# Performance work log

Hardware: AMD Instinct MI355X
Metric: run time of the kernel (lower is better)

Reference implementation:

```python
import jax, jax.numpy as jnp
import numpy as np

B, H = 65536, 512


def setup_inputs() -> dict:
    key = jax.random.key(0)
    ks = jax.random.split(key, 10)
    s = 1.0 / np.sqrt(H)  # torch nn.Linear default init range
    uni = lambda k, shape: jax.random.uniform(k, shape, jnp.float32, -s, s)
    return {
        "inputs": jax.random.normal(ks[0], (B, H), jnp.float32),
        "short_term_memory": jax.random.normal(ks[1], (B, H), jnp.float32),
        "Wf": uni(ks[2], (H, H)), "bf": uni(ks[3], (H,)),
        "Wi": uni(ks[4], (H, H)), "bi": uni(ks[5], (H,)),
        "Wg": uni(ks[6], (H, H)), "bg": uni(ks[7], (H,)),
        "Wo": uni(ks[8], (H, H)), "bo": uni(ks[9], (H,)),
    }


def reference(inputs, short_term_memory, Wf, bf, Wi, bi, Wg, bg, Wo, bo):
    z = inputs + short_term_memory  # [B, H]
    # ForgetGate: OVERWRITES long-term memory (previous cell state never read).
    c = jax.nn.sigmoid(z @ Wf.T + bf)
    # InputGate: c += sigmoid(...) * tanh(...)
    c = c + jax.nn.sigmoid(z @ Wi.T + bi) * jnp.tanh(z @ Wg.T + bg)
    # OutputGate: h = tanh(c) * sigmoid(...)
    h = jnp.tanh(c) * jax.nn.sigmoid(z @ Wo.T + bo)
    return jnp.stack((c, h))  # [2, B, H]: new long-term and short-term memory
```

## Files before the change

### kernel.cpp

```cpp
#include <hip/hip_runtime.h>

typedef __bf16 bf16x8 __attribute__((ext_vector_type(8)));
typedef float  f32x4  __attribute__((ext_vector_type(4)));

#define LOG2E 1.4426950408889634f

static __device__ __forceinline__ float fexp2(float x) { return __builtin_amdgcn_exp2f(x); }
static __device__ __forceinline__ float frcp(float x)  { return __builtin_amdgcn_rcpf(x); }
static __device__ __forceinline__ float fsigmoid(float x) { return frcp(1.0f + fexp2(-LOG2E * x)); }
static __device__ __forceinline__ float ftanh(float x)    { return 2.0f * frcp(1.0f + fexp2(-2.0f * LOG2E * x)) - 1.0f; }

__global__ __launch_bounds__(256) void wpack(const float* __restrict__ Wf,
                                             const float* __restrict__ Wi,
                                             const float* __restrict__ Wg,
                                             const float* __restrict__ Wo,
                                             __bf16* __restrict__ Wp)
{
    int idx = blockIdx.x * 256 + threadIdx.x;
    int kg  = idx & 63;
    int j   = (idx >> 6) & 511;
    int g   = idx >> 15;
    const float* src = (g == 0) ? Wf : (g == 1) ? Wi : (g == 2) ? Wg : Wo;
    const float4* s4 = (const float4*)(src + j * 512 + kg * 8);
    float4 v0 = s4[0], v1 = s4[1];
    bf16x8 o;
    o[0] = (__bf16)v0.x; o[1] = (__bf16)v0.y; o[2] = (__bf16)v0.z; o[3] = (__bf16)v0.w;
    o[4] = (__bf16)v1.x; o[5] = (__bf16)v1.y; o[6] = (__bf16)v1.z; o[7] = (__bf16)v1.w;
    int cn = j >> 4;
    int ks = kg >> 2;
    int lt = (j & 15) + (kg & 3) * 16;
    size_t dst = ((size_t)(((g * 32 + cn) * 16 + ks) * 64 + lt)) * 8;
    *(bf16x8*)(Wp + dst) = o;
}

__global__ __launch_bounds__(512, 2) void lstm_main(
    const float* __restrict__ xin, const float* __restrict__ stm,
    const __bf16* __restrict__ Wp,
    const float* __restrict__ bfv, const float* __restrict__ biv,
    const float* __restrict__ bgv, const float* __restrict__ bov,
    float* __restrict__ out)
{
    __shared__ unsigned char zs[131072];
    const int tid  = threadIdx.x;
    const int lane = tid & 63;
    const int wv   = tid >> 6;
    const int l15  = lane & 15;
    const int lq   = lane >> 4;
    const int row0 = blockIdx.x * 128;

    {
        const float* xb = xin + (size_t)row0 * 512;
        const float* sb = stm + (size_t)row0 * 512;
        #pragma unroll
        for (int it = 0; it < 16; ++it) {
            int idx = it * 512 + tid;
            int row = idx >> 6;
            int kg  = idx & 63;
            const float4* x4 = (const float4*)(xb + row * 512 + kg * 8);
            const float4* s4 = (const float4*)(sb + row * 512 + kg * 8);
            float4 a0 = x4[0], a1 = x4[1];
            float4 b0 = s4[0], b1 = s4[1];
            bf16x8 p;
            p[0] = (__bf16)(a0.x + b0.x); p[1] = (__bf16)(a0.y + b0.y);
            p[2] = (__bf16)(a0.z + b0.z); p[3] = (__bf16)(a0.w + b0.w);
            p[4] = (__bf16)(a1.x + b1.x); p[5] = (__bf16)(a1.y + b1.y);
            p[6] = (__bf16)(a1.z + b1.z); p[7] = (__bf16)(a1.w + b1.w);
            int rb   = row >> 5;
            int kk   = kg >> 1;
            int slot = ((row & 31) + (kg & 1) * 32) ^ (kk & 7);
            *(bf16x8*)(zs + rb * 32768 + kk * 1024 + slot * 16) = p;
        }
    }
    __syncthreads();

    const int kkoff = lq >> 1;
    const int s0    = l15 + (lq & 1) * 32;
    const int koffb = kkoff << 10;

    for (int ci = 0; ci < 4; ++ci) {
        const int cn   = ci * 8 + wv;
        const int colj = cn * 16 + l15;

        const __bf16* bp0 = Wp + ((size_t)((  0 + cn) * 16)) * 512 + lane * 8;
        const __bf16* bp1 = Wp + ((size_t)(( 32 + cn) * 16)) * 512 + lane * 8;
        const __bf16* bp2 = Wp + ((size_t)(( 64 + cn) * 16)) * 512 + lane * 8;
        const __bf16* bp3 = Wp + ((size_t)(( 96 + cn) * 16)) * 512 + lane * 8;

        float bias0 = bfv[colj], bias1 = biv[colj], bias2 = bgv[colj], bias3 = bov[colj];
        f32x4 acc[8][4];
        #pragma unroll
        for (int m = 0; m < 8; ++m) {
            #pragma unroll
            for (int r = 0; r < 4; ++r) {
                acc[m][0][r] = bias0; acc[m][1][r] = bias1;
                acc[m][2][r] = bias2; acc[m][3][r] = bias3;
            }
        }

        #pragma unroll 2
        for (int ks = 0; ks < 16; ++ks) {
            const int kk7 = ((2 * ks) & 7) | kkoff;
            const int t0  = ((s0 ^ kk7) << 4) + ks * 2048 + koffb;
            bf16x8 b0 = *(const bf16x8*)(bp0 + ks * 512);
            bf16x8 b1 = *(const bf16x8*)(bp1 + ks * 512);
            bf16x8 b2 = *(const bf16x8*)(bp2 + ks * 512);
            bf16x8 b3 = *(const bf16x8*)(bp3 + ks * 512);
            bf16x8 a[8];
            #pragma unroll
            for (int m = 0; m < 8; ++m)
                a[m] = *(const bf16x8*)(zs + (m >> 1) * 32768 + (m & 1) * 256 + t0);
            #pragma unroll
            for (int m = 0; m < 8; ++m) {
                acc[m][0] = __builtin_amdgcn_mfma_f32_16x16x32_bf16(a[m], b0, acc[m][0], 0, 0, 0);
                acc[m][1] = __builtin_amdgcn_mfma_f32_16x16x32_bf16(a[m], b1, acc[m][1], 0, 0, 0);
                acc[m][2] = __builtin_amdgcn_mfma_f32_16x16x32_bf16(a[m], b2, acc[m][2], 0, 0, 0);
                acc[m][3] = __builtin_amdgcn_mfma_f32_16x16x32_bf16(a[m], b3, acc[m][3], 0, 0, 0);
            }
        }

        #pragma unroll
        for (int m = 0; m < 8; ++m) {
            #pragma unroll
            for (int r = 0; r < 4; ++r) {
                float F = acc[m][0][r], I = acc[m][1][r];
                float G = acc[m][2][r], O = acc[m][3][r];
                float c = fsigmoid(F) + fsigmoid(I) * ftanh(G);
                float h = ftanh(c) * fsigmoid(O);
                int row = row0 + m * 16 + lq * 4 + r;
                int o   = row * 512 + colj;
                out[o] = c;
                out[33554432 + o] = h;
            }
        }
    }
}

extern "C" void kernel_launch(void* const* d_in, const int* in_sizes, int n_in,
                              void* d_out, int out_size, void* d_ws, size_t ws_size,
                              hipStream_t stream) {
    const float* xin = (const float*)d_in[0];
    const float* stm = (const float*)d_in[1];
    const float* Wf  = (const float*)d_in[2];
    const float* bf_ = (const float*)d_in[3];
    const float* Wi  = (const float*)d_in[4];
    const float* bi_ = (const float*)d_in[5];
    const float* Wg  = (const float*)d_in[6];
    const float* bg_ = (const float*)d_in[7];
    const float* Wo  = (const float*)d_in[8];
    const float* bo_ = (const float*)d_in[9];
    __bf16* Wp = (__bf16*)d_ws;

    wpack<<<512, 256, 0, stream>>>(Wf, Wi, Wg, Wo, Wp);
    lstm_main<<<512, 512, 0, stream>>>(xin, stm, Wp, bf_, bi_, bg_, bo_, (float*)d_out);
}
```

Baseline: 192.9 us.

## Split z packing into separate kernel and stream it into LDS via global_load_lds

Adds a zpack kernel that computes z = x + stm, converts it to bf16 and writes it in the swizzled LDS tile layout to a workspace buffer. The main kernel then copies each 128KB tile straight into LDS with global_load_lds, which removes the register-staged fp32 load/add/convert prologue. In exchange it adds an extra launch plus a 64MB bf16 write and read through global memory, on top of the original 256MB of fp32 input reads.

```diff
diff --git a/kernel.cpp b/kernel.cpp
--- a/kernel.cpp
+++ b/kernel.cpp
@@ -33,8 +33,39 @@
     *(bf16x8*)(Wp + dst) = o;
 }
 
+__global__ __launch_bounds__(512) void zpack(const float* __restrict__ x,
+                                             const float* __restrict__ s,
+                                             __bf16* __restrict__ zf)
+{
+    const int tid  = threadIdx.x;
+    const int lane = tid & 63;
+    const int wv   = tid >> 6;
+    const size_t tile = blockIdx.x;
+    const size_t row0 = tile * 128;
+    char* dstb = (char*)zf + tile * 131072;
+
+    #pragma unroll 4
+    for (int i = 0; i < 16; ++i) {
+        int c   = wv * 16 + i;
+        int rb  = c >> 5, kk = c & 31;
+        int rl  = rb * 32 + ((lane ^ (kk & 7)) & 31);
+        int kg  = 2 * kk + (lane >> 5);
+        size_t off = (row0 + rl) * 512 + kg * 8;
+        float4 a0 = *(const float4*)(x + off);
+        float4 a1 = *(const float4*)(x + off + 4);
+        float4 b0 = *(const float4*)(s + off);
+        float4 b1 = *(const float4*)(s + off + 4);
+        bf16x8 p;
+        p[0] = (__bf16)(a0.x + b0.x); p[1] = (__bf16)(a0.y + b0.y);
+        p[2] = (__bf16)(a0.z + b0.z); p[3] = (__bf16)(a0.w + b0.w);
+        p[4] = (__bf16)(a1.x + b1.x); p[5] = (__bf16)(a1.y + b1.y);
+        p[6] = (__bf16)(a1.z + b1.z); p[7] = (__bf16)(a1.w + b1.w);
+        *(bf16x8*)(dstb + c * 1024 + lane * 16) = p;
+    }
+}
+
 __global__ __launch_bounds__(512, 2) void lstm_main(
-    const float* __restrict__ xin, const float* __restrict__ stm,
+    const __bf16* __restrict__ zf,
     const __bf16* __restrict__ Wp,
     const float* __restrict__ bfv, const float* __restrict__ biv,
     const float* __restrict__ bgv, const float* __restrict__ bov,
@@ -49,28 +80,17 @@
     const int row0 = blockIdx.x * 128;
 
     {
-        const float* xb = xin + (size_t)row0 * 512;
-        const float* sb = stm + (size_t)row0 * 512;
+        const char* srcb = (const char*)zf + (size_t)blockIdx.x * 131072 + (size_t)lane * 16;
         #pragma unroll
-        for (int it = 0; it < 16; ++it) {
-            int idx = it * 512 + tid;
-            int row = idx >> 6;
-            int kg  = idx & 63;
-            const float4* x4 = (const float4*)(xb + row * 512 + kg * 8);
-            const float4* s4 = (const float4*)(sb + row * 512 + kg * 8);
-            float4 a0 = x4[0], a1 = x4[1];
-            float4 b0 = s4[0], b1 = s4[1];
-            bf16x8 p;
-            p[0] = (__bf16)(a0.x + b0.x); p[1] = (__bf16)(a0.y + b0.y);
-            p[2] = (__bf16)(a0.z + b0.z); p[3] = (__bf16)(a0.w + b0.w);
-            p[4] = (__bf16)(a1.x + b1.x); p[5] = (__bf16)(a1.y + b1.y);
-            p[6] = (__bf16)(a1.z + b1.z); p[7] = (__bf16)(a1.w + b1.w);
-            int rb   = row >> 5;
-            int kk   = kg >> 1;
-            int slot = ((row & 31) + (kg & 1) * 32) ^ (kk & 7);
-            *(bf16x8*)(zs + rb * 32768 + kk * 1024 + slot * 16) = p;
+        for (int i = 0; i < 16; ++i) {
+            int c = wv * 16 + i;
+            __builtin_amdgcn_global_load_lds(
+                (const __attribute__((address_space(1))) void*)(srcb + c * 1024),
+                (__attribute__((address_space(3))) void*)(zs + c * 1024),
+                16, 0, 0);
         }
     }
+    asm volatile("s_waitcnt vmcnt(0)");
     __syncthreads();
 
     const int kkoff = lq >> 1;
@@ -149,7 +169,9 @@
     const float* Wo  = (const float*)d_in[8];
     const float* bo_ = (const float*)d_in[9];
     __bf16* Wp = (__bf16*)d_ws;
+    __bf16* zf = (__bf16*)((char*)d_ws + (4 * 512 * 512 * 2));
 
     wpack<<<512, 256, 0, stream>>>(Wf, Wi, Wg, Wo, Wp);
-    lstm_main<<<512, 512, 0, stream>>>(xin, stm, Wp, bf_, bi_, bg_, bo_, (float*)d_out);
+    zpack<<<512, 512, 0, stream>>>(xin, stm, zf);
+    lstm_main<<<512, 512, 0, stream>>>(zf, Wp, bf_, bi_, bg_, bo_, (float*)d_out);
 }
```

Measured after the change: 243.3 us. +26.1%, slower.

## Interleave packed gate weights and double-buffer B-fragment loads across k-steps

Applied to the files above, without the earlier changes.

The packed weight layout is reordered so the four gate tiles for a given column block and k-step sit next to each other, letting each wave read them from one contiguous 4KB region. The k-loop is fully unrolled with two register sets of weight fragments, so the global loads for the next k-step are issued before the MFMAs of the current one. The aim is to hide global/L2 latency on the weight fragments behind matrix work. It costs extra VGPRs, which matters under the launch bound of 2 blocks per SM with large accumulator arrays.

```diff
diff --git a/kernel.cpp b/kernel.cpp
--- a/kernel.cpp
+++ b/kernel.cpp
@@ -29,7 +29,7 @@
     int cn = j >> 4;
     int ks = kg >> 2;
     int lt = (j & 15) + (kg & 3) * 16;
-    size_t dst = ((size_t)(((g * 32 + cn) * 16 + ks) * 64 + lt)) * 8;
+    size_t dst = ((size_t)(((cn * 16 + ks) * 4 + g) * 64 + lt)) * 8;
     *(bf16x8*)(Wp + dst) = o;
 }
 
@@ -77,14 +77,31 @@
     const int s0    = l15 + (lq & 1) * 32;
     const int koffb = kkoff << 10;
 
+#define LOADB(P, KS) { \
+    const __bf16* p_ = bp + (KS) * 2048; \
+    P##0 = *(const bf16x8*)(p_); \
+    P##1 = *(const bf16x8*)(p_ + 512); \
+    P##2 = *(const bf16x8*)(p_ + 1024); \
+    P##3 = *(const bf16x8*)(p_ + 1536); }
+#define DOMFMA(P, KS) { \
+    const int kk7_ = ((2 * (KS)) & 7) | kkoff; \
+    const int t0_  = ((s0 ^ kk7_) << 4) + (KS) * 2048 + koffb; \
+    bf16x8 a_[8]; \
+    _Pragma("unroll") \
+    for (int m = 0; m < 8; ++m) \
+        a_[m] = *(const bf16x8*)(zs + (m >> 1) * 32768 + (m & 1) * 256 + t0_); \
+    _Pragma("unroll") \
+    for (int m = 0; m < 8; ++m) { \
+        acc[m][0] = __builtin_amdgcn_mfma_f32_16x16x32_bf16(a_[m], P##0, acc[m][0], 0, 0, 0); \
+        acc[m][1] = __builtin_amdgcn_mfma_f32_16x16x32_bf16(a_[m], P##1, acc[m][1], 0, 0, 0); \
+        acc[m][2] = __builtin_amdgcn_mfma_f32_16x16x32_bf16(a_[m], P##2, acc[m][2], 0, 0, 0); \
+        acc[m][3] = __builtin_amdgcn_mfma_f32_16x16x32_bf16(a_[m], P##3, acc[m][3], 0, 0, 0); } }
+
     for (int ci = 0; ci < 4; ++ci) {
         const int cn   = ci * 8 + wv;
         const int colj = cn * 16 + l15;
 
-        const __bf16* bp0 = Wp + ((size_t)((  0 + cn) * 16)) * 512 + lane * 8;
-        const __bf16* bp1 = Wp + ((size_t)(( 32 + cn) * 16)) * 512 + lane * 8;
-        const __bf16* bp2 = Wp + ((size_t)(( 64 + cn) * 16)) * 512 + lane * 8;
-        const __bf16* bp3 = Wp + ((size_t)(( 96 + cn) * 16)) * 512 + lane * 8;
+        const __bf16* bp = Wp + (size_t)cn * 32768 + lane * 8;
 
         float bias0 = bfv[colj], bias1 = biv[colj], bias2 = bgv[colj], bias3 = bov[colj];
         f32x4 acc[8][4];
@@ -97,25 +114,16 @@
             }
         }
 
-        #pragma unroll 2
-        for (int ks = 0; ks < 16; ++ks) {
-            const int kk7 = ((2 * ks) & 7) | kkoff;
-            const int t0  = ((s0 ^ kk7) << 4) + ks * 2048 + koffb;
-            bf16x8 b0 = *(const bf16x8*)(bp0 + ks * 512);
-            bf16x8 b1 = *(const bf16x8*)(bp1 + ks * 512);
-            bf16x8 b2 = *(const bf16x8*)(bp2 + ks * 512);
-            bf16x8 b3 = *(const bf16x8*)(bp3 + ks * 512);
-            bf16x8 a[8];
-            #pragma unroll
-            for (int m = 0; m < 8; ++m)
-                a[m] = *(const bf16x8*)(zs + (m >> 1) * 32768 + (m & 1) * 256 + t0);
-            #pragma unroll
-            for (int m = 0; m < 8; ++m) {
-                acc[m][0] = __builtin_amdgcn_mfma_f32_16x16x32_bf16(a[m], b0, acc[m][0], 0, 0, 0);
-                acc[m][1] = __builtin_amdgcn_mfma_f32_16x16x32_bf16(a[m], b1, acc[m][1], 0, 0, 0);
-                acc[m][2] = __builtin_amdgcn_mfma_f32_16x16x32_bf16(a[m], b2, acc[m][2], 0, 0, 0);
-                acc[m][3] = __builtin_amdgcn_mfma_f32_16x16x32_bf16(a[m], b3, acc[m][3], 0, 0, 0);
-            }
+        bf16x8 bA0, bA1, bA2, bA3;
+        bf16x8 bB0, bB1, bB2, bB3;
+
+        LOADB(bA, 0)
+        #pragma unroll
+        for (int ks = 0; ks < 16; ks += 2) {
+            LOADB(bB, ks + 1)
+            DOMFMA(bA, ks)
+            if (ks + 2 < 16) LOADB(bA, ks + 2)
+            DOMFMA(bB, ks + 1)
         }
 
         #pragma unroll
@@ -133,6 +141,8 @@
             }
         }
     }
+#undef LOADB
+#undef DOMFMA
 }
 
 extern "C" void kernel_launch(void* const* d_in, const int* in_sizes, int n_in,
```

Result: slower. 707.8 us (+266.9%).

## Stream weight tiles into per-wave LDS double buffers via async global-to-LDS loads

Applied to the files above, without the earlier changes.

Weights are repacked so that all four gates for a given column block and k-step are contiguous. The main loop now fetches each k-step's B fragments with global_load_lds into a per-wave double-buffered LDS region, where they previously came from direct global loads into registers. Explicit vmcnt waits pipeline the next fetch against the current MFMAs, and s_setprio raises priority around the MFMA bursts. This grows LDS use to 160KB and relies on hand-placed waitcnt ordering, which adds hazard risk.

```diff
diff --git a/kernel.cpp b/kernel.cpp
--- a/kernel.cpp
+++ b/kernel.cpp
@@ -29,7 +29,7 @@
     int cn = j >> 4;
     int ks = kg >> 2;
     int lt = (j & 15) + (kg & 3) * 16;
-    size_t dst = ((size_t)(((g * 32 + cn) * 16 + ks) * 64 + lt)) * 8;
+    size_t dst = ((size_t)(((cn * 16 + ks) * 4 + g) * 64 + lt)) * 8;
     *(bf16x8*)(Wp + dst) = o;
 }
 
@@ -40,7 +40,8 @@
     const float* __restrict__ bgv, const float* __restrict__ bov,
     float* __restrict__ out)
 {
-    __shared__ unsigned char zs[131072];
+    __shared__ unsigned char lds[163840];
+    unsigned char* zs = lds;
     const int tid  = threadIdx.x;
     const int lane = tid & 63;
     const int wv   = tid >> 6;
@@ -74,19 +75,29 @@
     __syncthreads();
 
     const int kkoff = lq >> 1;
-    const int s0    = l15 + (lq & 1) * 32;
+    const int sl0   = l15 + (lq & 1) * 32;
     const int koffb = kkoff << 10;
+
+    unsigned char* bsw  = lds + 131072 + wv * 4096;
+    unsigned char* bswl = bsw + lane * 16;
+
+#define AS1(p) ((const __attribute__((address_space(1))) void*)(p))
+#define AS3(p) ((__attribute__((address_space(3))) void*)(p))
+#define ISSUE(IDX) { \
+    const char* s_ = wpB + (IDX) * 2048 + lane * 16; \
+    unsigned char* d_ = bsw + ((IDX) & 1) * 2048; \
+    __builtin_amdgcn_global_load_lds(AS1(s_), AS3(d_), 16, 0, 0); \
+    __builtin_amdgcn_global_load_lds(AS1(s_ + 1024), AS3(d_ + 1024), 16, 0, 0); }
+#define WAITV2 { asm volatile("s_waitcnt vmcnt(2)" ::: "memory"); __builtin_amdgcn_sched_barrier(0); }
+#define WAITV0 { asm volatile("s_waitcnt vmcnt(0)" ::: "memory"); __builtin_amdgcn_sched_barrier(0); }
 
     for (int ci = 0; ci < 4; ++ci) {
         const int cn   = ci * 8 + wv;
         const int colj = cn * 16 + l15;
+        const char* wpB = (const char*)Wp + (size_t)cn * 65536;
 
-        const __bf16* bp0 = Wp + ((size_t)((  0 + cn) * 16)) * 512 + lane * 8;
-        const __bf16* bp1 = Wp + ((size_t)(( 32 + cn) * 16)) * 512 + lane * 8;
-        const __bf16* bp2 = Wp + ((size_t)(( 64 + cn) * 16)) * 512 + lane * 8;
-        const __bf16* bp3 = Wp + ((size_t)(( 96 + cn) * 16)) * 512 + lane * 8;
-
-        float bias0 = bfv[colj], bias1 = biv[colj], bias2 = bgv[colj], bias3 = bov[colj];
+        float bias0 = bfv[colj], bias1 = biv[colj];
+        float bias2 = bgv[colj], bias3 = bov[colj];
         f32x4 acc[8][4];
         #pragma unroll
         for (int m = 0; m < 8; ++m) {
@@ -97,24 +108,42 @@
             }
         }
 
-        #pragma unroll 2
+        ISSUE(0)
+        #pragma unroll
         for (int ks = 0; ks < 16; ++ks) {
-            const int kk7 = ((2 * ks) & 7) | kkoff;
-            const int t0  = ((s0 ^ kk7) << 4) + ks * 2048 + koffb;
-            bf16x8 b0 = *(const bf16x8*)(bp0 + ks * 512);
-            bf16x8 b1 = *(const bf16x8*)(bp1 + ks * 512);
-            bf16x8 b2 = *(const bf16x8*)(bp2 + ks * 512);
-            bf16x8 b3 = *(const bf16x8*)(bp3 + ks * 512);
-            bf16x8 a[8];
-            #pragma unroll
-            for (int m = 0; m < 8; ++m)
-                a[m] = *(const bf16x8*)(zs + (m >> 1) * 32768 + (m & 1) * 256 + t0);
-            #pragma unroll
-            for (int m = 0; m < 8; ++m) {
-                acc[m][0] = __builtin_amdgcn_mfma_f32_16x16x32_bf16(a[m], b0, acc[m][0], 0, 0, 0);
-                acc[m][1] = __builtin_amdgcn_mfma_f32_16x16x32_bf16(a[m], b1, acc[m][1], 0, 0, 0);
-                acc[m][2] = __builtin_amdgcn_mfma_f32_16x16x32_bf16(a[m], b2, acc[m][2], 0, 0, 0);
-                acc[m][3] = __builtin_amdgcn_mfma_f32_16x16x32_bf16(a[m], b3, acc[m][3], 0, 0, 0);
+            ISSUE(2 * ks + 1)
+            WAITV2
+            bf16x8 a_[8];
+            {
+                const int kk7 = ((2 * ks) & 7) | kkoff;
+                const int t0  = ((sl0 ^ kk7) << 4) + ks * 2048 + koffb;
+                #pragma unroll
+                for (int m = 0; m < 8; ++m)
+                    a_[m] = *(const bf16x8*)(zs + (m >> 1) * 32768 + (m & 1) * 256 + t0);
+            }
+            {
+                bf16x8 b0 = *(const bf16x8*)(bswl);
+                bf16x8 b1 = *(const bf16x8*)(bswl + 1024);
+                __builtin_amdgcn_s_setprio(1);
+                #pragma unroll
+                for (int m = 0; m < 8; ++m) {
+                    acc[m][0] = __builtin_amdgcn_mfma_f32_16x16x32_bf16(a_[m], b0, acc[m][0], 0, 0, 0);
+                    acc[m][1] = __builtin_amdgcn_mfma_f32_16x16x32_bf16(a_[m], b1, acc[m][1], 0, 0, 0);
+                }
+                __builtin_amdgcn_s_setprio(0);
+            }
+            if (ks < 15) { ISSUE(2 * ks + 2) WAITV2 }
+            else         { WAITV0 }
+            {
+                bf16x8 b2 = *(const bf16x8*)(bswl + 2048);
+                bf16x8 b3 = *(const bf16x8*)(bswl + 3072);
+                __builtin_amdgcn_s_setprio(1);
+                #pragma unroll
+                for (int m = 0; m < 8; ++m) {
+                    acc[m][2] = __builtin_amdgcn_mfma_f32_16x16x32_bf16(a_[m], b2, acc[m][2], 0, 0, 0);
+                    acc[m][3] = __builtin_amdgcn_mfma_f32_16x16x32_bf16(a_[m], b3, acc[m][3], 0, 0, 0);
+                }
+                __builtin_amdgcn_s_setprio(0);
             }
         }
 
@@ -133,6 +162,11 @@
             }
         }
     }
+#undef ISSUE
+#undef WAITV2
+#undef WAITV0
+#undef AS1
+#undef AS3
 }
 
 extern "C" void kernel_launch(void* const* d_in, const int* in_sizes, int n_in,
```

New measurement: 190.4 us. No clear change (-1.3%).
